# Performance work log

Measured on AMD Instinct MI355X. Metric: run time of the kernel, lower is better.

Reference implementation:

```python
import jax, jax.numpy as jnp
import numpy as np

EPS = 1e-6


def _layernorm(x, g, b):
    mu = jnp.mean(x, axis=-1, keepdims=True)
    var = jnp.mean((x - mu) ** 2, axis=-1, keepdims=True)
    return (x - mu) * jax.lax.rsqrt(var + EPS) * g + b


def _sinusoidal_pe(seq_len, d_model):
    pos = jnp.arange(seq_len, dtype=jnp.float32)[:, None]
    div = jnp.exp(jnp.arange(0, d_model, 2, dtype=jnp.float32) * (-np.log(10000.0) / d_model))
    pe = jnp.zeros((seq_len, d_model), dtype=jnp.float32)
    pe = pe.at[:, 0::2].set(jnp.sin(pos * div))
    pe = pe.at[:, 1::2].set(jnp.cos(pos * div))
    return pe


def setup_inputs() -> dict:
    key = jax.random.key(0)
    ks = jax.random.split(key, 6)
    B, S, D, H = 4, 4096, 1024, 16
    std = 0.02
    return {
        "x": jax.random.normal(ks[0], (B, S, D), jnp.float32),
        "ln1_g": jnp.ones((D,), jnp.float32),
        "ln1_b": jnp.zeros((D,), jnp.float32),
        "w_qkv": jax.random.normal(ks[1], (D, 3 * D), jnp.float32) * std,
        "w_out": jax.random.normal(ks[2], (D, D), jnp.float32) * std,
        "b_out": jnp.zeros((D,), jnp.float32),
        "ln2_g": jnp.ones((D,), jnp.float32),
        "ln2_b": jnp.zeros((D,), jnp.float32),
        "w1": jax.random.normal(ks[3], (D, 2 * D), jnp.float32) * std,
        "b1": jnp.zeros((2 * D,), jnp.float32),
        "w2": jax.random.normal(ks[4], (2 * D, 2 * D), jnp.float32) * std,
        "b2": jnp.zeros((2 * D,), jnp.float32),
        "w3": jax.random.normal(ks[5], (2 * D, D), jnp.float32) * std,
        "b3": jnp.zeros((D,), jnp.float32),
    }


def reference(x, ln1_g, ln1_b, w_qkv, w_out, b_out, ln2_g, ln2_b, w1, b1, w2, b2, w3, b3):
    B, S, D = x.shape
    H = 16
    dh = D // H  # dim_head = 64

    h = _layernorm(x, ln1_g, ln1_b)
    h = h + _sinusoidal_pe(S, D)[None]  # space_dim == 1 -> sinusoidal PE

    # linear (kernelized, non-causal) self-attention: efficient-attention style
    qkv = h @ w_qkv  # [B,S,3D]
    q, k, v = jnp.split(qkv, 3, axis=-1)
    to_heads = lambda t: t.reshape(B, S, H, dh).transpose(0, 2, 1, 3)  # [B,H,S,dh]
    q, k, v = to_heads(q), to_heads(k), to_heads(v)
    q = jax.nn.softmax(q, axis=-1) * (dh ** -0.5)
    k = jax.nn.softmax(k, axis=2)  # softmax over sequence
    context = jnp.einsum('bhnd,bhne->bhde', k, v)  # [B,H,dh,dh]
    attn = jnp.einsum('bhnd,bhde->bhne', q, context)  # [B,H,S,dh]
    attn = attn.transpose(0, 2, 1, 3).reshape(B, S, D)
    attn = attn @ w_out + b_out

    x = x + attn  # residual (dropout p=0)

    y = _layernorm(x, ln2_g, ln2_b)
    y = jax.nn.gelu(y @ w1 + b1, approximate=False)
    y = jax.nn.gelu(y @ w2 + b2, approximate=False)
    y = y @ w3 + b3
    return x + y
```

## Files before the change

kernel.cpp:

```cpp
#include <hip/hip_runtime.h>
#include <cstdint>
#include <cstddef>

#define BB 4
#define SS 4096
#define DD 1024
#define HH 16
#define MM (BB*SS)

typedef __bf16 bf16x8 __attribute__((ext_vector_type(8)));
typedef float  f32x4  __attribute__((ext_vector_type(4)));

__device__ __forceinline__ float b2f(unsigned short h){
    union { unsigned int u; float f; } c; c.u = ((unsigned int)h) << 16; return c.f;
}
__device__ __forceinline__ float b2f_u(unsigned int u16){
    union { unsigned int u; float f; } c; c.u = u16 << 16; return c.f;
}
__device__ __forceinline__ unsigned short f2b(float f){
    union { float f; unsigned int u; } c; c.f = f;
    unsigned int u = c.u + 0x7FFFu + ((c.u >> 16) & 1u);
    return (unsigned short)(u >> 16);
}

__global__ void transpose_cvt(const float* __restrict__ src, unsigned short* __restrict__ dst,
                              int K, int N){
    __shared__ float tile[32][33];
    int kb = blockIdx.y*32, nb = blockIdx.x*32;
    int tx = threadIdx.x, ty = threadIdx.y;
    for(int i=0;i<32;i+=8) tile[ty+i][tx] = src[(size_t)(kb+ty+i)*N + nb+tx];
    __syncthreads();
    for(int i=0;i<32;i+=8) dst[(size_t)(nb+ty+i)*K + kb+tx] = f2b(tile[tx][ty+i]);
}

template<int INBF>
__global__ __launch_bounds__(256) void ln_kernel(const void* __restrict__ xin,
                                                 const float* __restrict__ g,
                                                 const float* __restrict__ bta,
                                                 unsigned short* __restrict__ out,
                                                 int add_pe){
    int row = blockIdx.x;
    int t = threadIdx.x;
    float4 v;
    if (INBF == 0) {
        v = ((const float4*)((const float*)xin + (size_t)row*DD))[t];
    } else {
        ushort4 u = ((const ushort4*)((const unsigned short*)xin + (size_t)row*DD))[t];
        v.x = b2f(u.x); v.y = b2f(u.y); v.z = b2f(u.z); v.w = b2f(u.w);
    }
    float s = v.x+v.y+v.z+v.w;
    float q = v.x*v.x+v.y*v.y+v.z*v.z+v.w*v.w;
    for(int off=32; off>0; off>>=1){ s += __shfl_xor(s, off); q += __shfl_xor(q, off); }
    __shared__ float red[8];
    int wv = t>>6, ln = t&63;
    if(ln==0){ red[wv] = s; red[4+wv] = q; }
    __syncthreads();
    s = red[0]+red[1]+red[2]+red[3];
    q = red[4]+red[5]+red[6]+red[7];
    float mu = s * (1.0f/1024.0f);
    float var = q * (1.0f/1024.0f) - mu*mu;
    float rs = rsqrtf(var + 1e-6f);
    int d0 = t*4;
    float4 gg = ((const float4*)g)[t];
    float4 bb = ((const float4*)bta)[t];
    float o0 = (v.x-mu)*rs*gg.x + bb.x;
    float o1 = (v.y-mu)*rs*gg.y + bb.y;
    float o2 = (v.z-mu)*rs*gg.z + bb.z;
    float o3 = (v.w-mu)*rs*gg.w + bb.w;
    if(add_pe){
        int sidx = row & (SS-1);
        const float cfac = -0.008994473019508968f;
        float a0 = (float)sidx * expf(cfac * (float)(d0));
        float a1 = (float)sidx * expf(cfac * (float)(d0 + 2));
        o0 += sinf(a0); o1 += cosf(a0);
        o2 += sinf(a1); o3 += cosf(a1);
    }
    ushort4 o;
    o.x = f2b(o0); o.y = f2b(o1); o.z = f2b(o2); o.w = f2b(o3);
    *(ushort4*)(out + (size_t)row*DD + d0) = o;
}

template<int EPI>
__global__ __launch_bounds__(256, 2) void gemm_bt(
        const unsigned short* __restrict__ A,
        const unsigned short* __restrict__ Bt,
        void* __restrict__ Cout,
        const float* __restrict__ bias,
        const void* __restrict__ resid,
        int M, int N, int K)
{
    __shared__ __align__(16) unsigned short lA[128*64];
    __shared__ __align__(16) unsigned short lB[128*64];
    const int tid  = threadIdx.x;
    const int lane = tid & 63;
    const int wave = tid >> 6;
    const int quad = lane >> 4;
    const int l16  = lane & 15;
    const int wr = wave >> 1, wc = wave & 1;

    int gn  = gridDim.x;
    int lin = blockIdx.y * gn + blockIdx.x;
    int xcd = lin & 7;
    int j   = lin >> 3;
    int mt  = xcd + 8*(j/gn);
    int nt  = j - (j/gn)*gn;
    const int m0 = mt * 128;
    const int n0 = nt * 128;

    f32x4 acc[4][4] = {};

    for (int k0 = 0; k0 < K; k0 += 64) {
        __syncthreads();
        #pragma unroll
        for (int i = 0; i < 4; i++) {
            int c   = tid + 256*i;
            int row = c >> 3;
            int kc  = ((c & 7) ^ (row & 7)) << 3;
            const unsigned short* gA = A  + (size_t)(m0 + row) * K + k0 + kc;
            const unsigned short* gB = Bt + (size_t)(n0 + row) * K + k0 + kc;
            char* lpA = ((char*)lA) + (wave<<10) + (i<<12);
            char* lpB = ((char*)lB) + (wave<<10) + (i<<12);
            __builtin_amdgcn_global_load_lds((const __attribute__((address_space(1))) void*)gA,
                                             (__attribute__((address_space(3))) void*)lpA, 16, 0, 0);
            __builtin_amdgcn_global_load_lds((const __attribute__((address_space(1))) void*)gB,
                                             (__attribute__((address_space(3))) void*)lpB, 16, 0, 0);
        }
        __syncthreads();
        #pragma unroll
        for (int kk = 0; kk < 2; kk++) {
            bf16x8 af[4], bfr[4];
            #pragma unroll
            for (int mi = 0; mi < 4; mi++) {
                int row = wr*64 + mi*16 + l16;
                int kb  = (kk*64 + quad*16) ^ ((row & 7) << 4);
                af[mi] = *(const bf16x8*)((const char*)lA + row*128 + kb);
            }
            #pragma unroll
            for (int ni = 0; ni < 4; ni++) {
                int row = wc*64 + ni*16 + l16;
                int kb  = (kk*64 + quad*16) ^ ((row & 7) << 4);
                bfr[ni] = *(const bf16x8*)((const char*)lB + row*128 + kb);
            }
            #pragma unroll
            for (int mi = 0; mi < 4; mi++)
                #pragma unroll
                for (int ni = 0; ni < 4; ni++)
                    acc[mi][ni] = __builtin_amdgcn_mfma_f32_16x16x32_bf16(af[mi], bfr[ni], acc[mi][ni], 0, 0, 0);
        }
    }

    #pragma unroll
    for (int mi = 0; mi < 4; mi++) {
        #pragma unroll
        for (int r = 0; r < 4; r++) {
            int grow = m0 + wr*64 + mi*16 + quad*4 + r;
            #pragma unroll
            for (int ni = 0; ni < 4; ni++) {
                int gcol = n0 + wc*64 + ni*16 + l16;
                float v = acc[mi][ni][r];
                size_t idx = (size_t)grow * N + gcol;
                if (EPI == 0) {
                    ((unsigned short*)Cout)[idx] = f2b(v);
                } else if (EPI == 1) {
                    v += bias[gcol];
                    v = 0.5f * v * (1.0f + erff(v * 0.70710678118654752f));
                    ((unsigned short*)Cout)[idx] = f2b(v);
                } else if (EPI == 2) {
                    v += bias[gcol] + ((const float*)resid)[idx];
                    ((unsigned short*)Cout)[idx] = f2b(v);
                } else {
                    v += bias[gcol] + b2f(((const unsigned short*)resid)[idx]);
                    ((float*)Cout)[idx] = v;
                }
            }
        }
    }
}

__global__ __launch_bounds__(256) void ctx_partial(const unsigned short* __restrict__ qkv,
                                                   float* __restrict__ EP,
                                                   float* __restrict__ CS){
    int sc = blockIdx.x, h = blockIdx.y, b = blockIdx.z;
    int t = threadIdx.x;
    __shared__ __align__(16) float kl[64][64];
    __shared__ __align__(16) float vl[64][64];
    __shared__ float csred[4][64];
    float acc[4][4] = {};
    float cspart = 0.0f;
    int e4 = (t & 15) * 4, d4 = (t >> 4) * 4;
    int dcol = t & 63, schunk = t >> 6;
    for(int s0 = 0; s0 < 256; s0 += 64){
        __syncthreads();
        #pragma unroll
        for(int j=0;j<2;j++){
            int lin = t + 256*j;
            int row = lin >> 3;
            int c8  = (lin & 7) * 8;
            size_t gr = (size_t)(b*SS + sc*256 + s0 + row);
            uint4 kv = *(const uint4*)(qkv + gr*3072 + DD + h*64 + c8);
            float4 ka, kb2;
            ka.x = expf(b2f_u(kv.x & 0xFFFFu)); ka.y = expf(b2f_u(kv.x >> 16));
            ka.z = expf(b2f_u(kv.y & 0xFFFFu)); ka.w = expf(b2f_u(kv.y >> 16));
            kb2.x = expf(b2f_u(kv.z & 0xFFFFu)); kb2.y = expf(b2f_u(kv.z >> 16));
            kb2.z = expf(b2f_u(kv.w & 0xFFFFu)); kb2.w = expf(b2f_u(kv.w >> 16));
            *(float4*)&kl[row][c8]   = ka;
            *(float4*)&kl[row][c8+4] = kb2;
            uint4 vv = *(const uint4*)(qkv + gr*3072 + 2*DD + h*64 + c8);
            float4 va, vb;
            va.x = b2f_u(vv.x & 0xFFFFu); va.y = b2f_u(vv.x >> 16);
            va.z = b2f_u(vv.y & 0xFFFFu); va.w = b2f_u(vv.y >> 16);
            vb.x = b2f_u(vv.z & 0xFFFFu); vb.y = b2f_u(vv.z >> 16);
            vb.z = b2f_u(vv.w & 0xFFFFu); vb.w = b2f_u(vv.w >> 16);
            *(float4*)&vl[row][c8]   = va;
            *(float4*)&vl[row][c8+4] = vb;
        }
        __syncthreads();
        #pragma unroll
        for(int i=0;i<16;i++) cspart += kl[schunk*16+i][dcol];
        for(int s=0;s<64;s++){
            float4 k4 = *(const float4*)&kl[s][d4];
            float4 v4 = *(const float4*)&vl[s][e4];
            acc[0][0] += k4.x*v4.x; acc[0][1] += k4.x*v4.y; acc[0][2] += k4.x*v4.z; acc[0][3] += k4.x*v4.w;
            acc[1][0] += k4.y*v4.x; acc[1][1] += k4.y*v4.y; acc[1][2] += k4.y*v4.z; acc[1][3] += k4.y*v4.w;
            acc[2][0] += k4.z*v4.x; acc[2][1] += k4.z*v4.y; acc[2][2] += k4.z*v4.z; acc[2][3] += k4.z*v4.w;
            acc[3][0] += k4.w*v4.x; acc[3][1] += k4.w*v4.y; acc[3][2] += k4.w*v4.z; acc[3][3] += k4.w*v4.w;
        }
    }
    int slot = (b*HH + h)*16 + sc;
    float* ep = EP + (size_t)slot*4096;
    #pragma unroll
    for(int i=0;i<4;i++)
        *(float4*)&ep[(d4+i)*64 + e4] = *(float4*)&acc[i][0];
    csred[schunk][dcol] = cspart;
    __syncthreads();
    if(t < 64) CS[slot*64 + t] = csred[0][t]+csred[1][t]+csred[2][t]+csred[3][t];
}

__global__ __launch_bounds__(256) void ctx_reduce(const float* __restrict__ EP,
                                                  const float* __restrict__ CS,
                                                  float* __restrict__ CTXF){
    int bh = blockIdx.x;
    int t = threadIdx.x;
    int d = t >> 2, e0 = (t & 3) * 16;
    float cs = 0.0f;
    #pragma unroll
    for(int sl=0; sl<16; sl++) cs += CS[(bh*16+sl)*64 + d];
    float inv = 1.0f/cs;
    #pragma unroll
    for(int i=0;i<16;i++){
        float s = 0.0f;
        #pragma unroll
        for(int sl=0; sl<16; sl++) s += EP[(size_t)(bh*16+sl)*4096 + d*64 + e0 + i];
        CTXF[(size_t)bh*4096 + d*64 + e0 + i] = s * inv;
    }
}

__global__ __launch_bounds__(256) void attn_heads(const unsigned short* __restrict__ qkv,
                                                  const float* __restrict__ CTXF,
                                                  unsigned short* __restrict__ abuf){
    int rg = blockIdx.x, h = blockIdx.y;
    int b = rg >> 6;
    int t = threadIdx.x;
    __shared__ __align__(16) float cl[64][64];
    __shared__ __align__(16) float qlT[64*68];
    const float* cb = CTXF + (size_t)(b*HH + h)*4096;
    for(int j=0;j<4;j++){
        int lin = t + 256*j;
        ((float4*)cl)[lin] = ((const float4*)cb)[lin];
    }
    {
        int r = t >> 2, seg = (t & 3) * 16;
        const unsigned short* qp = qkv + (size_t)(rg*64 + r)*3072 + h*64 + seg;
        float vals[16];
        float m = -1e30f;
        #pragma unroll
        for(int u=0; u<4; u++){
            ushort4 qv = *(const ushort4*)(qp + u*4);
            vals[u*4+0]=b2f(qv.x); vals[u*4+1]=b2f(qv.y); vals[u*4+2]=b2f(qv.z); vals[u*4+3]=b2f(qv.w);
        }
        #pragma unroll
        for(int i=0;i<16;i++) m = fmaxf(m, vals[i]);
        m = fmaxf(m, __shfl_xor(m, 1));
        m = fmaxf(m, __shfl_xor(m, 2));
        float ssum = 0.0f;
        #pragma unroll
        for(int i=0;i<16;i++){ vals[i] = expf(vals[i]-m); ssum += vals[i]; }
        ssum += __shfl_xor(ssum, 1);
        ssum += __shfl_xor(ssum, 2);
        float scl = 0.125f/ssum;
        #pragma unroll
        for(int i=0;i<16;i++) qlT[(seg+i)*68 + r] = vals[i]*scl;
    }
    __syncthreads();
    int e4 = (t & 15) * 4, r4 = (t >> 4) * 4;
    float acc[4][4] = {};
    for(int d=0; d<64; d++){
        float4 q4 = *(const float4*)&qlT[d*68 + r4];
        float4 c4 = *(const float4*)&cl[d][e4];
        acc[0][0] += q4.x*c4.x; acc[0][1] += q4.x*c4.y; acc[0][2] += q4.x*c4.z; acc[0][3] += q4.x*c4.w;
        acc[1][0] += q4.y*c4.x; acc[1][1] += q4.y*c4.y; acc[1][2] += q4.y*c4.z; acc[1][3] += q4.y*c4.w;
        acc[2][0] += q4.z*c4.x; acc[2][1] += q4.z*c4.y; acc[2][2] += q4.z*c4.z; acc[2][3] += q4.z*c4.w;
        acc[3][0] += q4.w*c4.x; acc[3][1] += q4.w*c4.y; acc[3][2] += q4.w*c4.z; acc[3][3] += q4.w*c4.w;
    }
    #pragma unroll
    for(int i=0;i<4;i++){
        ushort4 o;
        o.x = f2b(acc[i][0]); o.y = f2b(acc[i][1]); o.z = f2b(acc[i][2]); o.w = f2b(acc[i][3]);
        *(ushort4*)(abuf + (size_t)(rg*64 + r4 + i)*DD + h*64 + e4) = o;
    }
}

extern "C" void kernel_launch(void* const* d_in, const int* in_sizes, int n_in,
                              void* d_out, int out_size, void* d_ws, size_t ws_size,
                              hipStream_t stream)
{
    const float* x     = (const float*)d_in[0];
    const float* ln1_g = (const float*)d_in[1];
    const float* ln1_b = (const float*)d_in[2];
    const float* w_qkv = (const float*)d_in[3];
    const float* w_out = (const float*)d_in[4];
    const float* b_out = (const float*)d_in[5];
    const float* ln2_g = (const float*)d_in[6];
    const float* ln2_b = (const float*)d_in[7];
    const float* w1    = (const float*)d_in[8];
    const float* b1    = (const float*)d_in[9];
    const float* w2    = (const float*)d_in[10];
    const float* b2    = (const float*)d_in[11];
    const float* w3    = (const float*)d_in[12];
    const float* b3    = (const float*)d_in[13];

    char* ws = (char*)d_ws;
    unsigned short* wqkvT = (unsigned short*)(ws + 0);
    unsigned short* woutT = (unsigned short*)(ws + 6291456);
    unsigned short* w1T   = (unsigned short*)(ws + 8388608);
    unsigned short* w2T   = (unsigned short*)(ws + 12582912);
    unsigned short* w3T   = (unsigned short*)(ws + 20971520);
    unsigned short* Hbuf  = (unsigned short*)(ws + 25165824);
    unsigned short* QKV   = (unsigned short*)(ws + 58720256);
    float*          EP    = (float*)(ws + 159383552);
    float*          CS    = (float*)(ws + 176160768);
    float*          CTXF  = (float*)(ws + 176422912);
    unsigned short* Abuf  = Hbuf;
    unsigned short* X2    = (unsigned short*)(ws + 58720256);
    unsigned short* H2    = Hbuf;
    unsigned short* Y1    = (unsigned short*)d_out;
    unsigned short* Y2    = (unsigned short*)(ws + 125829120);

    dim3 tb(32, 8);
    transpose_cvt<<<dim3(3072/32, 1024/32), tb, 0, stream>>>(w_qkv, wqkvT, 1024, 3072);
    transpose_cvt<<<dim3(1024/32, 1024/32), tb, 0, stream>>>(w_out, woutT, 1024, 1024);
    transpose_cvt<<<dim3(2048/32, 1024/32), tb, 0, stream>>>(w1,    w1T,   1024, 2048);
    transpose_cvt<<<dim3(2048/32, 2048/32), tb, 0, stream>>>(w2,    w2T,   2048, 2048);
    transpose_cvt<<<dim3(1024/32, 2048/32), tb, 0, stream>>>(w3,    w3T,   2048, 1024);

    ln_kernel<0><<<MM, 256, 0, stream>>>(x, ln1_g, ln1_b, Hbuf, 1);

    gemm_bt<0><<<dim3(3072/128, MM/128), 256, 0, stream>>>(Hbuf, wqkvT, QKV, nullptr, nullptr, MM, 3072, 1024);

    ctx_partial<<<dim3(16, HH, BB), 256, 0, stream>>>(QKV, EP, CS);
    ctx_reduce<<<BB*HH, 256, 0, stream>>>(EP, CS, CTXF);
    attn_heads<<<dim3(256, HH), 256, 0, stream>>>(QKV, CTXF, Abuf);

    gemm_bt<2><<<dim3(1024/128, MM/128), 256, 0, stream>>>(Abuf, woutT, X2, b_out, x, MM, 1024, 1024);

    ln_kernel<1><<<MM, 256, 0, stream>>>(X2, ln2_g, ln2_b, H2, 0);

    gemm_bt<1><<<dim3(2048/128, MM/128), 256, 0, stream>>>(H2, w1T, Y1, b1, nullptr, MM, 2048, 1024);
    gemm_bt<1><<<dim3(2048/128, MM/128), 256, 0, stream>>>(Y1, w2T, Y2, b2, nullptr, MM, 2048, 2048);
    gemm_bt<3><<<dim3(1024/128, MM/128), 256, 0, stream>>>(Y2, w3T, d_out, b3, X2, MM, 1024, 2048);
}
```

Measured before the change: 721.7 us.

## Replace 128x128 GEMM with double-buffered 256x256 ping-pong pipelined kernel

Replaces the simple 128x128 tile GEMM, which synchronises on every 64-wide K step, with a 256x256 tile, 512-thread kernel. It double-buffers LDS, interleaves async global-to-LDS staging with MFMA quadrants, and uses explicit waitcnt, barriers and setprio to overlap memory with compute. Larger tiles raise data reuse per block. In exchange, LDS use per block grows (128 KB) and register pressure rises, and the hand-tuned waitcnt counts are fragile.

Result: slower. 745.8 us (+3.3%).

```diff
diff --git a/kernel.cpp b/kernel.cpp
--- a/kernel.cpp
+++ b/kernel.cpp
@@ -80,8 +80,54 @@
     *(ushort4*)(out + (size_t)row*DD + d0) = o;
 }
 
+
+#define BARX __builtin_amdgcn_s_barrier()
+#define LGK0 { asm volatile("s_waitcnt lgkmcnt(0)" ::: "memory"); __builtin_amdgcn_sched_barrier(0); }
+#define LGK8 asm volatile("s_waitcnt lgkmcnt(8)" ::: "memory")
+#define VM6  asm volatile("s_waitcnt vmcnt(6)" ::: "memory")
+#define PRIO1 __builtin_amdgcn_s_setprio(1)
+#define PRIO0 __builtin_amdgcn_s_setprio(0)
+
+#define LDA(D, QR) { \
+    const char* _pa = sA + (((D)*2+(QR))<<14) + rbaseA; \
+    _Pragma("unroll") \
+    for (int mi = 0; mi < 4; mi++) { \
+        ra[mi][0] = *(const bf16x8*)(_pa + (mi<<11) + kb0); \
+        ra[mi][1] = *(const bf16x8*)(_pa + (mi<<11) + kb1); \
+    } }
+
+#define LDB(RB, D, QC) { \
+    const char* _pb = sB + (((D)*2+(QC))<<14) + rbaseB; \
+    _Pragma("unroll") \
+    for (int nj = 0; nj < 2; nj++) { \
+        RB[nj][0] = *(const bf16x8*)(_pb + (nj<<11) + kb0); \
+        RB[nj][1] = *(const bf16x8*)(_pb + (nj<<11) + kb1); \
+    } }
+
+#define MMAC(RB, QR, QC) { \
+    _Pragma("unroll") \
+    for (int mi = 0; mi < 4; mi++) \
+    _Pragma("unroll") \
+    for (int nj = 0; nj < 2; nj++) \
+    _Pragma("unroll") \
+    for (int kk = 0; kk < 2; kk++) \
+        acc[(QR)*4+mi][(QC)*2+nj] = __builtin_amdgcn_mfma_f32_16x16x32_bf16( \
+            ra[mi][kk], RB[nj][kk], acc[(QR)*4+mi][(QC)*2+nj], 0, 0, 0); }
+
+#define STAGEA(D, H, KS) { \
+    __builtin_amdgcn_global_load_lds((const __attribute__((address_space(1))) void*)(pA[H][0] + (KS)), \
+        (__attribute__((address_space(3))) void*)(sA + (((D)*2+(H))<<14) + wbase), 16, 0, 0); \
+    __builtin_amdgcn_global_load_lds((const __attribute__((address_space(1))) void*)(pA[H][1] + (KS)), \
+        (__attribute__((address_space(3))) void*)(sA + (((D)*2+(H))<<14) + wbase + 8192), 16, 0, 0); }
+
+#define STAGEB(D, Q, KS) { \
+    __builtin_amdgcn_global_load_lds((const __attribute__((address_space(1))) void*)(pB[Q][0] + (KS)), \
+        (__attribute__((address_space(3))) void*)(sB + (((D)*2+(Q))<<14) + wbase), 16, 0, 0); \
+    __builtin_amdgcn_global_load_lds((const __attribute__((address_space(1))) void*)(pB[Q][1] + (KS)), \
+        (__attribute__((address_space(3))) void*)(sB + (((D)*2+(Q))<<14) + wbase + 8192), 16, 0, 0); }
+
 template<int EPI>
-__global__ __launch_bounds__(256, 2) void gemm_bt(
+__global__ __launch_bounds__(512, 2) void gemm256(
         const unsigned short* __restrict__ A,
         const unsigned short* __restrict__ Bt,
         void* __restrict__ Cout,
@@ -89,14 +135,18 @@
         const void* __restrict__ resid,
         int M, int N, int K)
 {
-    __shared__ __align__(16) unsigned short lA[128*64];
-    __shared__ __align__(16) unsigned short lB[128*64];
+    __shared__ __align__(16) unsigned short lAbuf[2*2*128*64];
+    __shared__ __align__(16) unsigned short lBbuf[2*2*128*64];
+    char* sA = (char*)lAbuf;
+    char* sB = (char*)lBbuf;
+
     const int tid  = threadIdx.x;
     const int lane = tid & 63;
     const int wave = tid >> 6;
     const int quad = lane >> 4;
     const int l16  = lane & 15;
-    const int wr = wave >> 1, wc = wave & 1;
+    const int wr = wave >> 2;
+    const int wc = wave & 3;
 
     int gn  = gridDim.x;
     int lin = blockIdx.y * gn + blockIdx.x;
@@ -104,60 +154,84 @@
     int j   = lin >> 3;
     int mt  = xcd + 8*(j/gn);
     int nt  = j - (j/gn)*gn;
-    const int m0 = mt * 128;
-    const int n0 = nt * 128;
-
-    f32x4 acc[4][4] = {};
-
-    for (int k0 = 0; k0 < K; k0 += 64) {
-        __syncthreads();
-        #pragma unroll
-        for (int i = 0; i < 4; i++) {
-            int c   = tid + 256*i;
-            int row = c >> 3;
-            int kc  = ((c & 7) ^ (row & 7)) << 3;
-            const unsigned short* gA = A  + (size_t)(m0 + row) * K + k0 + kc;
-            const unsigned short* gB = Bt + (size_t)(n0 + row) * K + k0 + kc;
-            char* lpA = ((char*)lA) + (wave<<10) + (i<<12);
-            char* lpB = ((char*)lB) + (wave<<10) + (i<<12);
-            __builtin_amdgcn_global_load_lds((const __attribute__((address_space(1))) void*)gA,
-                                             (__attribute__((address_space(3))) void*)lpA, 16, 0, 0);
-            __builtin_amdgcn_global_load_lds((const __attribute__((address_space(1))) void*)gB,
-                                             (__attribute__((address_space(3))) void*)lpB, 16, 0, 0);
+    const int m0 = mt * 256;
+    const int n0 = nt * 256;
+
+    const unsigned short* pA[2][2];
+    const unsigned short* pB[2][2];
+    #pragma unroll
+    for (int h = 0; h < 2; h++) {
+        #pragma unroll
+        for (int jj = 0; jj < 2; jj++) {
+            int c  = tid + 512*jj;
+            int lr = c >> 3;
+            int kc = ((c & 7) ^ (lr & 7)) << 3;
+            int ga = m0 + ((lr>>6)<<7) + h*64 + (lr & 63);
+            int gb = n0 + ((lr>>5)<<6) + h*32 + (lr & 31);
+            pA[h][jj] = A  + (size_t)ga * K + kc;
+            pB[h][jj] = Bt + (size_t)gb * K + kc;
         }
-        __syncthreads();
-        #pragma unroll
-        for (int kk = 0; kk < 2; kk++) {
-            bf16x8 af[4], bfr[4];
-            #pragma unroll
-            for (int mi = 0; mi < 4; mi++) {
-                int row = wr*64 + mi*16 + l16;
-                int kb  = (kk*64 + quad*16) ^ ((row & 7) << 4);
-                af[mi] = *(const bf16x8*)((const char*)lA + row*128 + kb);
-            }
-            #pragma unroll
-            for (int ni = 0; ni < 4; ni++) {
-                int row = wc*64 + ni*16 + l16;
-                int kb  = (kk*64 + quad*16) ^ ((row & 7) << 4);
-                bfr[ni] = *(const bf16x8*)((const char*)lB + row*128 + kb);
-            }
-            #pragma unroll
-            for (int mi = 0; mi < 4; mi++)
-                #pragma unroll
-                for (int ni = 0; ni < 4; ni++)
-                    acc[mi][ni] = __builtin_amdgcn_mfma_f32_16x16x32_bf16(af[mi], bfr[ni], acc[mi][ni], 0, 0, 0);
-        }
-    }
-
-    #pragma unroll
-    for (int mi = 0; mi < 4; mi++) {
+    }
+    const int wbase  = wave << 10;
+    const int rbaseA = (wr*64 + l16) * 128;
+    const int rbaseB = (wc*32 + l16) * 128;
+    const int kb0 = (quad*16)      ^ ((l16 & 7) << 4);
+    const int kb1 = (64 + quad*16) ^ ((l16 & 7) << 4);
+
+    f32x4 acc[8][4] = {};
+    bf16x8 ra[4][2], rb0[2][2], rb1[2][2];
+
+    STAGEA(0,0, 0); STAGEB(0,0, 0); STAGEB(0,1, 0); STAGEA(0,1, 0);
+    STAGEA(1,0, 64); STAGEB(1,0, 64); STAGEB(1,1, 64);
+    VM6;
+    BARX;
+
+    const int NIT = K >> 7;
+    for (int it = 0; it < NIT; it++) {
+        int ka  = it << 7;
+        int kb_ = ka + 64;
+        int kc2 = ka + 128; if (kc2 >= K) kc2 = 0;
+        int kc3 = ka + 192; if (kc3 >= K) kc3 = 0;
+
+        LDA(0,0); LDB(rb0, 0,0);
+        STAGEA(1,1, kb_);
+        LGK8;
+        BARX; LGK0; PRIO1; MMAC(rb0, 0,0); PRIO0; BARX;
+        LDB(rb1, 0,1);
+        STAGEA(0,0, kc2);
+        BARX; LGK0; PRIO1; MMAC(rb1, 0,1); PRIO0; BARX;
+        LDA(0,1);
+        STAGEB(0,0, kc2);
+        BARX; LGK0; PRIO1; MMAC(rb1, 1,1); PRIO0; BARX;
+        STAGEB(0,1, kc2);
+        VM6;
+        BARX; LGK0; PRIO1; MMAC(rb0, 1,0); PRIO0; BARX;
+        LDA(1,0); LDB(rb0, 1,0);
+        STAGEA(0,1, kc2);
+        LGK8;
+        BARX; LGK0; PRIO1; MMAC(rb0, 0,0); PRIO0; BARX;
+        LDB(rb1, 1,1);
+        STAGEA(1,0, kc3);
+        BARX; LGK0; PRIO1; MMAC(rb1, 0,1); PRIO0; BARX;
+        LDA(1,1);
+        STAGEB(1,0, kc3);
+        BARX; LGK0; PRIO1; MMAC(rb1, 1,1); PRIO0; BARX;
+        STAGEB(1,1, kc3);
+        VM6;
+        BARX; LGK0; PRIO1; MMAC(rb0, 1,0); PRIO0; BARX;
+    }
+    asm volatile("s_waitcnt vmcnt(0)" ::: "memory");
+
+    #pragma unroll
+    for (int qm = 0; qm < 8; qm++) {
+        int grow0 = m0 + wr*128 + (qm>>2)*64 + (qm&3)*16 + quad*4;
         #pragma unroll
         for (int r = 0; r < 4; r++) {
-            int grow = m0 + wr*64 + mi*16 + quad*4 + r;
+            int grow = grow0 + r;
             #pragma unroll
             for (int ni = 0; ni < 4; ni++) {
                 int gcol = n0 + wc*64 + ni*16 + l16;
-                float v = acc[mi][ni][r];
+                float v = acc[qm][ni][r];
                 size_t idx = (size_t)grow * N + gcol;
                 if (EPI == 0) {
                     ((unsigned short*)Cout)[idx] = f2b(v);
@@ -355,17 +429,17 @@
 
     ln_kernel<0><<<MM, 256, 0, stream>>>(x, ln1_g, ln1_b, Hbuf, 1);
 
-    gemm_bt<0><<<dim3(3072/128, MM/128), 256, 0, stream>>>(Hbuf, wqkvT, QKV, nullptr, nullptr, MM, 3072, 1024);
+    gemm256<0><<<dim3(3072/256, MM/256), 512, 0, stream>>>(Hbuf, wqkvT, QKV, nullptr, nullptr, MM, 3072, 1024);
 
     ctx_partial<<<dim3(16, HH, BB), 256, 0, stream>>>(QKV, EP, CS);
     ctx_reduce<<<BB*HH, 256, 0, stream>>>(EP, CS, CTXF);
     attn_heads<<<dim3(256, HH), 256, 0, stream>>>(QKV, CTXF, Abuf);
 
-    gemm_bt<2><<<dim3(1024/128, MM/128), 256, 0, stream>>>(Abuf, woutT, X2, b_out, x, MM, 1024, 1024);
+    gemm256<2><<<dim3(1024/256, MM/256), 512, 0, stream>>>(Abuf, woutT, X2, b_out, x, MM, 1024, 1024);
 
     ln_kernel<1><<<MM, 256, 0, stream>>>(X2, ln2_g, ln2_b, H2, 0);
 
-    gemm_bt<1><<<dim3(2048/128, MM/128), 256, 0, stream>>>(H2, w1T, Y1, b1, nullptr, MM, 2048, 1024);
-    gemm_bt<1><<<dim3(2048/128, MM/128), 256, 0, stream>>>(Y1, w2T, Y2, b2, nullptr, MM, 2048, 2048);
-    gemm_bt<3><<<dim3(1024/128, MM/128), 256, 0, stream>>>(Y2, w3T, d_out, b3, X2, MM, 1024, 2048);
-}
+    gemm256<1><<<dim3(2048/256, MM/256), 512, 0, stream>>>(H2, w1T, Y1, b1, nullptr, MM, 2048, 1024);
+    gemm256<1><<<dim3(2048/256, MM/256), 512, 0, stream>>>(Y1, w2T, Y2, b2, nullptr, MM, 2048, 2048);
+    gemm256<3><<<dim3(1024/256, MM/256), 512, 0, stream>>>(Y2, w3T, d_out, b3, X2, MM, 1024, 2048);
+}
```
